# Kernel optimization log

Measured on AMD Instinct MI355X. Metric: run time of the kernel, lower is better.

## Reference

```python
import jax, jax.numpy as jnp
import numpy as np
import math

NUM_HEADS = 16
HEAD_DIM = 128
ROPE_BASE = 10000.0


def setup_inputs() -> dict:
    key = jax.random.key(0)
    ks = jax.random.split(key, 6)
    B, S, H = 2, 2048, 2048
    hidden_states = jax.random.normal(ks[0], (B, S, H), dtype=jnp.float32) * 0.02
    # causal additive mask, shape (B, 1, S, S)
    neg = jnp.finfo(jnp.float32).min
    causal = jnp.where(jnp.tril(jnp.ones((S, S), dtype=bool)), 0.0, neg).astype(jnp.float32)
    attention_mask = jnp.broadcast_to(causal[None, None], (B, 1, S, S))
    position_ids = jnp.broadcast_to(jnp.arange(S, dtype=jnp.int64)[None], (B, S))
    scale = 1.0 / math.sqrt(H)
    Wq = jax.random.normal(ks[1], (H, H), dtype=jnp.float32) * scale
    Wk = jax.random.normal(ks[2], (H, H), dtype=jnp.float32) * scale
    Wv = jax.random.normal(ks[3], (H, H), dtype=jnp.float32) * scale
    Wo = jax.random.normal(ks[4], (H, H), dtype=jnp.float32) * scale
    return {"hidden_states": hidden_states, "attention_mask": attention_mask,
            "position_ids": position_ids, "Wq": Wq, "Wk": Wk, "Wv": Wv, "Wo": Wo}


def _rotate_half(x):
    x1, x2 = jnp.split(x, 2, axis=-1)
    return jnp.concatenate((-x2, x1), axis=-1)


def reference(hidden_states, attention_mask, position_ids, Wq, Wk, Wv, Wo):
    B, S, H = hidden_states.shape
    nh, hd = NUM_HEADS, HEAD_DIM

    def shape_heads(x):  # (B,S,H) -> (B,nh,S,hd)
        return x.reshape(B, S, nh, hd).transpose(0, 2, 1, 3)

    q = shape_heads(hidden_states @ Wq.T)
    k = shape_heads(hidden_states @ Wk.T)
    v = shape_heads(hidden_states @ Wv.T)

    kv_seq_len = S  # no past_key_value
    # rotary table: (kv_seq_len, hd)
    inv_freq = 1.0 / (ROPE_BASE ** (jnp.arange(0, hd, 2, dtype=jnp.float32) / hd))
    t = jnp.arange(kv_seq_len, dtype=jnp.float32)
    freqs = jnp.einsum('i,j->ij', t, inv_freq)
    emb = jnp.concatenate((freqs, freqs), axis=-1)
    # gather-based RoPE == table lookup at position_ids: (B,S,hd) -> (B,1,S,hd)
    cos = jnp.cos(emb)[position_ids][:, None]
    sin = jnp.sin(emb)[position_ids][:, None]

    q = q * cos + _rotate_half(q) * sin
    k = k * cos + _rotate_half(k) * sin

    scores = jnp.einsum('bhqd,bhkd->bhqk', q, k) / math.sqrt(hd)
    scores = scores + attention_mask
    scores = jnp.maximum(scores, jnp.finfo(scores.dtype).min)
    probs = jax.nn.softmax(scores.astype(jnp.float32), axis=-1).astype(q.dtype)
    attn = jnp.einsum('bhqk,bhkd->bhqd', probs, v)  # (B,nh,S,hd)
    attn = attn.transpose(0, 2, 1, 3).reshape(B, S, H)
    return attn @ Wo.T
```

## Files before the change

kernel.cpp:

```cpp
#include <hip/hip_runtime.h>
#include <hip/hip_bf16.h>
#include <cstdint>

#define SQ    2048
#define HDIM  2048
#define NH    16
#define HD    128
#define BATCH 2
#define MTOK  (BATCH*SQ)

typedef unsigned short u16;
typedef unsigned int   u32;
typedef __bf16 bf16x8 __attribute__((ext_vector_type(8)));
typedef float  f32x4  __attribute__((ext_vector_type(4)));
typedef float  f32x16 __attribute__((ext_vector_type(16)));
typedef unsigned short u16x4 __attribute__((ext_vector_type(4)));
typedef unsigned int   u32x4 __attribute__((ext_vector_type(4)));

__device__ __forceinline__ u16 f2b(float f) {
  union { float f; unsigned u; } v; v.f = f;
  return (u16)((v.u + 0x7fffu + ((v.u >> 16) & 1u)) >> 16);
}
__device__ __forceinline__ float b2f(u16 b) {
  union { unsigned u; float f; } v; v.u = ((unsigned)b) << 16;
  return v.f;
}

#define GLD_LDS16(gp, lp) __builtin_amdgcn_global_load_lds( \
    (const __attribute__((address_space(1))) uint32_t*)(gp), \
    (__attribute__((address_space(3))) uint32_t*)(lp), 16, 0, 0)

__device__ __forceinline__ f32x16 zero16() {
  f32x16 v;
#pragma unroll
  for (int i = 0; i < 16; ++i) v[i] = 0.f;
  return v;
}

__global__ __launch_bounds__(256) void conv_bf16(const float* __restrict__ in,
                                                 u16* __restrict__ out, int n4) {
  int i = blockIdx.x * 256 + threadIdx.x;
  if (i >= n4) return;
  float4 v = ((const float4*)in)[i];
  u16x4 o;
  o.x = f2b(v.x); o.y = f2b(v.y); o.z = f2b(v.z); o.w = f2b(v.w);
  *(u16x4*)(out + (size_t)i * 4) = o;
}

__global__ __launch_bounds__(256) void conv_w4(const float* __restrict__ w0,
                                               const float* __restrict__ w1,
                                               const float* __restrict__ w2,
                                               const float* __restrict__ w3,
                                               u16* o0, u16* o1, u16* o2, u16* o3) {
  int i = blockIdx.x * 256 + threadIdx.x;
  int sel = blockIdx.y;
  const float* in = sel == 0 ? w0 : sel == 1 ? w1 : sel == 2 ? w2 : w3;
  u16* out = sel == 0 ? o0 : sel == 1 ? o1 : sel == 2 ? o2 : o3;
  float4 v = ((const float4*)in)[i];
  u16x4 o;
  o.x = f2b(v.x); o.y = f2b(v.y); o.z = f2b(v.z); o.w = f2b(v.w);
  *(u16x4*)(out + (size_t)i * 4) = o;
}

__global__ void rope_table_k(float* __restrict__ ct, float* __restrict__ st) {
  int s = blockIdx.x, j = threadIdx.x;
  float invf = expf(-(float)j * (9.210340371976184f / 64.0f));
  float ang = (float)s * invf;
  ct[s * 64 + j] = cosf(ang);
  st[s * 64 + j] = sinf(ang);
}

__global__ __launch_bounds__(256) void rope_apply2(u16* __restrict__ Xq,
                                                   u16* __restrict__ Xk,
                                                   const float* __restrict__ ct,
                                                   const float* __restrict__ st) {
  u16* X = blockIdx.y ? Xk : Xq;
  int idx = blockIdx.x * 256 + threadIdx.x;
  int j = idx & 63;
  int row = idx >> 6;
  int s = row & (SQ - 1);
  size_t base = (size_t)row * HD;
  float x1 = b2f(X[base + j]), x2 = b2f(X[base + j + 64]);
  float c = ct[s * 64 + j], sn = st[s * 64 + j];
  X[base + j]      = f2b(x1 * c - x2 * sn);
  X[base + j + 64] = f2b(x2 * c + x1 * sn);
}

template<int BM, int OUT>
__global__ __launch_bounds__(512, 2)
void gemm8(const u16* __restrict__ A, const u16* __restrict__ W0,
           const u16* __restrict__ W1, const u16* __restrict__ W2,
           u16* __restrict__ oQ, u16* __restrict__ oK, u16* __restrict__ oV,
           float* __restrict__ oF) {
  constexpr int ALT = BM / 64;
  constexpr int TLT = ALT + 4;
  constexpr int MF  = BM / 32;
  constexpr int MPP = MF / 4;
  __shared__ u16 Asb[2][BM * 64];
  __shared__ u16 Bsb[2][256 * 64];
  const int tid = threadIdx.x, lane = tid & 63, w = tid >> 6;
  const int wm = w >> 2, wn = w & 3;
  const int gx = gridDim.x;
  const int lin = blockIdx.y * gx + blockIdx.x;
  const int cpx = (gx * gridDim.y) >> 3;
  const int swz = (lin & 7) * cpx + (lin >> 3);
  const int bx = swz % gx, by = swz / gx;
  const int m0 = by * BM;
  const int n0g = bx * 256;
  int sel; const u16* Bw; int nloc;
  if (OUT == 0) {
    sel = n0g >> 11;
    Bw = (sel == 0) ? W0 : (sel == 1) ? W1 : W2;
    nloc = n0g & 2047;
  } else {
    sel = 0; Bw = W0; nloc = n0g;
  }

  size_t aoff[ALT]; int aldso[ALT];
  size_t boff[4];   int bldso[4];
#pragma unroll
  for (int i = 0; i < ALT; ++i) {
    int c = i * 512 + tid, r = c >> 3, sl = c & 7;
    aoff[i] = (size_t)(m0 + r) * HDIM + ((sl ^ (r & 7)) * 8);
    aldso[i] = (i * 512 + w * 64) * 8;
  }
#pragma unroll
  for (int i = 0; i < 4; ++i) {
    int c = i * 512 + tid, r = c >> 3, sl = c & 7;
    boff[i] = (size_t)(nloc + r) * HDIM + ((sl ^ (r & 7)) * 8);
    bldso[i] = (i * 512 + w * 64) * 8;
  }
  auto stage = [&](int buf, int k0) {
#pragma unroll
    for (int i = 0; i < ALT; ++i) GLD_LDS16(A + aoff[i] + k0, &Asb[buf][aldso[i]]);
#pragma unroll
    for (int i = 0; i < 4; ++i) GLD_LDS16(Bw + boff[i] + k0, &Bsb[buf][bldso[i]]);
  };

  f32x4 acc[MF][4];
#pragma unroll
  for (int i = 0; i < MF; ++i)
#pragma unroll
    for (int j = 0; j < 4; ++j) acc[i][j] = (f32x4){0.f, 0.f, 0.f, 0.f};

  const int l15 = lane & 15, hi4 = lane >> 4;
  const int swr = (l15 & 7) << 4;

  stage(0, 0);

  const int NT = HDIM / 64;
  for (int t = 0; t < NT; ++t) {
    const int cur = t & 1;
    if (t + 1 < NT) {
      stage(cur ^ 1, (t + 1) * 64);
      if constexpr (BM == 256) asm volatile("s_waitcnt vmcnt(8)" ::: "memory");
      else                     asm volatile("s_waitcnt vmcnt(6)" ::: "memory");
    } else {
      asm volatile("s_waitcnt vmcnt(0)" ::: "memory");
    }
    __builtin_amdgcn_s_barrier();

    const char* Ab = (const char*)Asb[cur];
    const char* Bb = (const char*)Bsb[cur];

    bf16x8 bfr[4][2];
#pragma unroll
    for (int ni = 0; ni < 4; ++ni)
#pragma unroll
      for (int kk = 0; kk < 2; ++kk)
        bfr[ni][kk] = *(const bf16x8*)(Bb + (wn * 64 + ni * 16 + l15) * 128 +
                                       ((kk * 64 + hi4 * 16) ^ swr));
    bf16x8 afA[MPP][2], afB[MPP][2];
    auto lda = [&](bf16x8 (&dst)[MPP][2], int pp) {
#pragma unroll
      for (int j = 0; j < MPP; ++j)
#pragma unroll
        for (int kk = 0; kk < 2; ++kk)
          dst[j][kk] = *(const bf16x8*)(Ab + (wm * (BM / 2) + (pp * MPP + j) * 16 + l15) * 128 +
                                        ((kk * 64 + hi4 * 16) ^ swr));
    };
    auto mf = [&](bf16x8 (&af)[MPP][2], int pp) {
#pragma unroll
      for (int kk = 0; kk < 2; ++kk)
#pragma unroll
        for (int j = 0; j < MPP; ++j)
#pragma unroll
          for (int ni = 0; ni < 4; ++ni)
            acc[pp * MPP + j][ni] = __builtin_amdgcn_mfma_f32_16x16x32_bf16(
                af[j][kk], bfr[ni][kk], acc[pp * MPP + j][ni], 0, 0, 0);
    };

    lda(afA, 0);
    asm volatile("s_waitcnt lgkmcnt(0)" ::: "memory");
    __builtin_amdgcn_sched_barrier(0);
    lda(afB, 1);
    __builtin_amdgcn_s_setprio(1); mf(afA, 0); __builtin_amdgcn_s_setprio(0);
    asm volatile("s_waitcnt lgkmcnt(0)" ::: "memory");
    __builtin_amdgcn_sched_barrier(0);
    lda(afA, 2);
    __builtin_amdgcn_s_setprio(1); mf(afB, 1); __builtin_amdgcn_s_setprio(0);
    asm volatile("s_waitcnt lgkmcnt(0)" ::: "memory");
    __builtin_amdgcn_sched_barrier(0);
    lda(afB, 3);
    __builtin_amdgcn_s_setprio(1); mf(afA, 2); __builtin_amdgcn_s_setprio(0);
    asm volatile("s_waitcnt lgkmcnt(0)" ::: "memory");
    __builtin_amdgcn_sched_barrier(0);
    __builtin_amdgcn_s_setprio(1); mf(afB, 3); __builtin_amdgcn_s_setprio(0);
    __builtin_amdgcn_s_barrier();
  }

  const int cl = l15, rg = hi4 * 4;
#pragma unroll
  for (int mi = 0; mi < MF; ++mi) {
#pragma unroll
    for (int ni = 0; ni < 4; ++ni) {
      const int mb = m0 + wm * (BM / 2) + mi * 16 + rg;
      const int n = nloc + wn * 64 + ni * 16 + cl;
      if (OUT == 1) {
#pragma unroll
        for (int r = 0; r < 4; ++r)
          oF[(size_t)(mb + r) * HDIM + n] = acc[mi][ni][r];
      } else {
        const int h = n >> 7, d = n & 127;
        if (sel == 2) {
          const int b = mb >> 11, s = mb & (SQ - 1);
          u16x4 pk;
          pk.x = f2b(acc[mi][ni][0]); pk.y = f2b(acc[mi][ni][1]);
          pk.z = f2b(acc[mi][ni][2]); pk.w = f2b(acc[mi][ni][3]);
          *(u16x4*)&oV[((size_t)(b * NH + h) * HD + d) * SQ + s] = pk;
        } else {
          u16* O = sel ? oK : oQ;
#pragma unroll
          for (int r = 0; r < 4; ++r) {
            const int m = mb + r, b = m >> 11, s = m & (SQ - 1);
            O[((size_t)(b * NH + h) * SQ + s) * HD + d] = f2b(acc[mi][ni][r]);
          }
        }
      }
    }
  }
}

__device__ __forceinline__ void stage_kv(u16* ksb, u16* vsb,
                                         const u16* __restrict__ Kg,
                                         const u16* __restrict__ Vg,
                                         int kv0, int w, int lane) {
#pragma unroll
  for (int i = 0; i < 4; ++i) {
    int chunk = (w * 4 + i) * 64 + lane;
    int row = chunk >> 4, c16 = chunk & 15;
    int csrc = c16 ^ (row & 7);
    GLD_LDS16(Kg + (size_t)(kv0 + row) * HD + csrc * 8, ksb + (w * 4 + i) * 512);
  }
#pragma unroll
  for (int i = 0; i < 4; ++i) {
    int chunk = (w * 4 + i) * 64 + lane;
    int d = chunk >> 3, c8 = chunk & 7;
    int csrc = c8 ^ (d & 7);
    GLD_LDS16(Vg + (size_t)d * SQ + kv0 + csrc * 8, vsb + (w * 4 + i) * 512);
  }
}

#define MKPA(dst, P, off) { \
  u32 u0_, u1_, u2_, u3_; \
  asm("v_cvt_pk_bf16_f32 %0, %1, %2" : "=v"(u0_) : "v"(P[off + 0]), "v"(P[off + 1])); \
  asm("v_cvt_pk_bf16_f32 %0, %1, %2" : "=v"(u1_) : "v"(P[off + 2]), "v"(P[off + 3])); \
  asm("v_cvt_pk_bf16_f32 %0, %1, %2" : "=v"(u2_) : "v"(P[off + 4]), "v"(P[off + 5])); \
  asm("v_cvt_pk_bf16_f32 %0, %1, %2" : "=v"(u3_) : "v"(P[off + 6]), "v"(P[off + 7])); \
  u32 x0_ = (u32)__shfl_xor((int)u0_, 32, 64); \
  u32 x1_ = (u32)__shfl_xor((int)u1_, 32, 64); \
  u32 x2_ = (u32)__shfl_xor((int)u2_, 32, 64); \
  u32 x3_ = (u32)__shfl_xor((int)u3_, 32, 64); \
  u32x4 w_; \
  w_.x = hi ? x2_ : u0_; \
  w_.y = hi ? x3_ : u1_; \
  w_.z = hi ? u2_ : x0_; \
  w_.w = hi ? u3_ : x1_; \
  dst = __builtin_bit_cast(bf16x8, w_); \
}

#define PVD(oD, dblk) { \
  const int dr_ = (dblk) * 32 + l31; \
  const int sw_ = (dr_ & 7) << 4; \
  bf16x8 v0_ = *(const bf16x8*)(Vb + ((dr_ * 128 +  0 + hi * 16) ^ sw_)); \
  oD = __builtin_amdgcn_mfma_f32_32x32x16_bf16(pa[0], v0_, oD, 0, 0, 0); \
  bf16x8 v1_ = *(const bf16x8*)(Vb + ((dr_ * 128 + 32 + hi * 16) ^ sw_)); \
  oD = __builtin_amdgcn_mfma_f32_32x32x16_bf16(pa[1], v1_, oD, 0, 0, 0); \
  bf16x8 v2_ = *(const bf16x8*)(Vb + ((dr_ * 128 + 64 + hi * 16) ^ sw_)); \
  oD = __builtin_amdgcn_mfma_f32_32x32x16_bf16(pa[2], v2_, oD, 0, 0, 0); \
  bf16x8 v3_ = *(const bf16x8*)(Vb + ((dr_ * 128 + 96 + hi * 16) ^ sw_)); \
  oD = __builtin_amdgcn_mfma_f32_32x32x16_bf16(pa[3], v3_, oD, 0, 0, 0); \
}

__global__ __launch_bounds__(256, 2)
void flash_fwd2(const u16* __restrict__ Q, const u16* __restrict__ K,
                const u16* __restrict__ Vt, u16* __restrict__ Out) {
  __shared__ u16 Ks[2][64 * 128];
  __shared__ u16 Vs[2][128 * 64];
  const int tid = threadIdx.x, lane = tid & 63, w = tid >> 6;
  const int hi = lane >> 5, l31 = lane & 31;
  const int qt = 15 - (int)(blockIdx.x >> 5);
  const int bh = blockIdx.x & 31;
  const int q0 = qt * 128;
  const u16* Qg = Q + (size_t)bh * SQ * HD;
  const u16* Kg = K + (size_t)bh * SQ * HD;
  const u16* Vg = Vt + (size_t)bh * HD * SQ;
  const int qw = q0 + w * 32;
  const int qg = qw + l31;

  bf16x8 qf[8];
#pragma unroll
  for (int st = 0; st < 8; ++st)
    qf[st] = *(const bf16x8*)&Qg[(size_t)qg * HD + st * 16 + hi * 8];

  f32x16 o0 = zero16(), o1 = zero16(), o2 = zero16(), o3 = zero16();
  float lsum = 0.f;
  const float sL2E = 0.1275174446f;
  const int ktl = 2 * qt + 1;
  int cur = 0;

  stage_kv(Ks[0], Vs[0], Kg, Vg, 0, w, lane);

  for (int kt = 0; kt <= ktl; ++kt) {
    if (kt < ktl) {
      stage_kv(Ks[cur ^ 1], Vs[cur ^ 1], Kg, Vg, (kt + 1) * 64, w, lane);
      asm volatile("s_waitcnt vmcnt(8)" ::: "memory");
    } else {
      asm volatile("s_waitcnt vmcnt(0)" ::: "memory");
    }
    __builtin_amdgcn_s_barrier();

    const int kv0 = kt * 64;
    if (kv0 <= qw + 31) {
      const char* Kb = (const char*)Ks[cur];
      const char* Vb = (const char*)Vs[cur];
      f32x16 c0 = zero16(), c1 = zero16();
      const int kr0 = l31, kr1 = 32 + l31;
      const int sw0 = (kr0 & 7) << 4;
#pragma unroll
      for (int st = 0; st < 8; ++st) {
        bf16x8 k0 = *(const bf16x8*)(Kb + ((kr0 * 256 + st * 32 + hi * 16) ^ sw0));
        c0 = __builtin_amdgcn_mfma_f32_32x32x16_bf16(k0, qf[st], c0, 0, 0, 0);
        bf16x8 k1 = *(const bf16x8*)(Kb + ((kr1 * 256 + st * 32 + hi * 16) ^ sw0));
        c1 = __builtin_amdgcn_mfma_f32_32x32x16_bf16(k1, qf[st], c1, 0, 0, 0);
      }
      const bool needmask = (kv0 + 63 > qw);
      const int lim0 = qg - kv0, lim1 = lim0 - 32;
      if (needmask) {
#pragma unroll
        for (int r = 0; r < 16; ++r) {
          const int cr = (r & 3) + 8 * (r >> 2) + 4 * hi;
          float p0 = exp2f(c0[r] * sL2E);
          c0[r] = (cr <= lim0) ? p0 : 0.f;
          float p1 = exp2f(c1[r] * sL2E);
          c1[r] = (cr <= lim1) ? p1 : 0.f;
          lsum += c0[r] + c1[r];
        }
      } else {
#pragma unroll
        for (int r = 0; r < 16; ++r) {
          c0[r] = exp2f(c0[r] * sL2E);
          c1[r] = exp2f(c1[r] * sL2E);
          lsum += c0[r] + c1[r];
        }
      }
      bf16x8 pa[4];
      MKPA(pa[0], c0, 0); MKPA(pa[1], c0, 8);
      MKPA(pa[2], c1, 0); MKPA(pa[3], c1, 8);
      PVD(o0, 0) PVD(o1, 1) PVD(o2, 2) PVD(o3, 3)
    }
    __builtin_amdgcn_s_barrier();
    cur ^= 1;
  }

  float ltot = lsum + __shfl_xor(lsum, 32, 64);
  float invl = 1.f / ltot;
  const int b = bh >> 4, h = bh & 15;
#pragma unroll
  for (int g = 0; g < 4; ++g) {
#pragma unroll
    for (int j = 0; j < 4; ++j) {
      const int r = g * 4 + j;
      const int cr = g * 8 + 4 * hi + j;
      float inv = __shfl(invl, cr, 64);
      const int s = q0 + w * 32 + cr;
      size_t rb = ((size_t)(b * SQ + s)) * HDIM + h * HD;
      Out[rb +  0 + l31] = f2b(o0[r] * inv);
      Out[rb + 32 + l31] = f2b(o1[r] * inv);
      Out[rb + 64 + l31] = f2b(o2[r] * inv);
      Out[rb + 96 + l31] = f2b(o3[r] * inv);
    }
  }
}

extern "C" void kernel_launch(void* const* d_in, const int* in_sizes, int n_in,
                              void* d_out, int out_size, void* d_ws, size_t ws_size,
                              hipStream_t stream) {
  const float* hs = (const float*)d_in[0];
  const float* Wq = (const float*)d_in[3];
  const float* Wk = (const float*)d_in[4];
  const float* Wv = (const float*)d_in[5];
  const float* Wo = (const float*)d_in[6];

  char* ws = (char*)d_ws;
  u16* XB  = (u16*)(ws);
  u16* WQB = (u16*)(ws + (size_t)(16 << 20));
  u16* WKB = (u16*)(ws + (size_t)(24 << 20));
  u16* WVB = (u16*)(ws + (size_t)(32 << 20));
  u16* WOB = (u16*)(ws + (size_t)(40 << 20));
  u16* QR  = (u16*)(ws + (size_t)(48 << 20));
  u16* KR  = (u16*)(ws + (size_t)(64 << 20));
  u16* VT  = (u16*)(ws + (size_t)(80 << 20));
  u16* ATT = (u16*)(ws + (size_t)(96 << 20));
  float* CT = (float*)(ws + (size_t)(112 << 20));
  float* ST = (float*)(ws + (size_t)(112 << 20) + (1 << 19));

  conv_bf16<<<8192, 256, 0, stream>>>(hs, XB, 2097152);
  conv_w4<<<dim3(4096, 4), 256, 0, stream>>>(Wq, Wk, Wv, Wo, WQB, WKB, WVB, WOB);
  rope_table_k<<<SQ, 64, 0, stream>>>(CT, ST);

  gemm8<256, 0><<<dim3(24, 16), 512, 0, stream>>>(XB, WQB, WKB, WVB,
                                                  QR, KR, VT, nullptr);

  rope_apply2<<<dim3(16384, 2), 256, 0, stream>>>(QR, KR, CT, ST);

  flash_fwd2<<<512, 256, 0, stream>>>(QR, KR, VT, ATT);

  gemm8<128, 1><<<dim3(8, 32), 512, 0, stream>>>(ATT, WOB, nullptr, nullptr,
                                                 nullptr, nullptr, nullptr,
                                                 (float*)d_out);
}
```

Baseline: 291.2 us.

## Split GEMM tiles into half-buffers with four-phase staggered load/compute pipeline

Rewrites the GEMM main loop so the A and B tiles are each split into two halves in shared memory. Each K-step runs four phases, and every phase issues the global-to-LDS load for one half of the next tile while computing on one quadrant of the current tile. The aim is finer-grained overlap of memory traffic with MFMA work and more even spreading of vmcnt waits. In exchange it adds a barrier per phase and makes the waitcnt bookkeeping more complex.

```diff
diff --git a/kernel.cpp b/kernel.cpp
--- a/kernel.cpp
+++ b/kernel.cpp
@@ -88,16 +88,17 @@
 
 template<int BM, int OUT>
 __global__ __launch_bounds__(512, 2)
-void gemm8(const u16* __restrict__ A, const u16* __restrict__ W0,
-           const u16* __restrict__ W1, const u16* __restrict__ W2,
-           u16* __restrict__ oQ, u16* __restrict__ oK, u16* __restrict__ oV,
-           float* __restrict__ oF) {
-  constexpr int ALT = BM / 64;
-  constexpr int TLT = ALT + 4;
+void gemm8j(const u16* __restrict__ A, const u16* __restrict__ W0,
+            const u16* __restrict__ W1, const u16* __restrict__ W2,
+            u16* __restrict__ oQ, u16* __restrict__ oK, u16* __restrict__ oV,
+            float* __restrict__ oF) {
   constexpr int MF  = BM / 32;
-  constexpr int MPP = MF / 4;
-  __shared__ u16 Asb[2][BM * 64];
-  __shared__ u16 Bsb[2][256 * 64];
+  constexpr int MH  = MF / 2;
+  constexpr int WU  = BM / 4;
+  constexpr int WUS = (BM == 256) ? 6 : 5;
+  constexpr int ALH = BM / 128;
+  __shared__ u16 Ah[2][2][(BM / 2) * 64];
+  __shared__ u16 Bh[2][2][128 * 64];
   const int tid = threadIdx.x, lane = tid & 63, w = tid >> 6;
   const int wm = w >> 2, wn = w & 3;
   const int gx = gridDim.x;
@@ -116,25 +117,31 @@
     sel = 0; Bw = W0; nloc = n0g;
   }
 
-  size_t aoff[ALT]; int aldso[ALT];
-  size_t boff[4];   int bldso[4];
-#pragma unroll
-  for (int i = 0; i < ALT; ++i) {
-    int c = i * 512 + tid, r = c >> 3, sl = c & 7;
-    aoff[i] = (size_t)(m0 + r) * HDIM + ((sl ^ (r & 7)) * 8);
-    aldso[i] = (i * 512 + w * 64) * 8;
-  }
-#pragma unroll
-  for (int i = 0; i < 4; ++i) {
-    int c = i * 512 + tid, r = c >> 3, sl = c & 7;
-    boff[i] = (size_t)(nloc + r) * HDIM + ((sl ^ (r & 7)) * 8);
-    bldso[i] = (i * 512 + w * 64) * 8;
-  }
-  auto stage = [&](int buf, int k0) {
-#pragma unroll
-    for (int i = 0; i < ALT; ++i) GLD_LDS16(A + aoff[i] + k0, &Asb[buf][aldso[i]]);
-#pragma unroll
-    for (int i = 0; i < 4; ++i) GLD_LDS16(Bw + boff[i] + k0, &Bsb[buf][bldso[i]]);
+  u32 aoff[2][ALH], boff[2][2];
+#pragma unroll
+  for (int h = 0; h < 2; ++h) {
+#pragma unroll
+    for (int l = 0; l < ALH; ++l) {
+      int c = l * 512 + tid, ra = c >> 3, sl = c & 7;
+      int r = ((ra >> WUS) << (WUS + 1)) + h * WU + (ra & (WU - 1));
+      aoff[h][l] = (u32)((m0 + r) * HDIM + ((sl ^ (ra & 7)) * 8));
+    }
+#pragma unroll
+    for (int l = 0; l < 2; ++l) {
+      int c = l * 512 + tid, cb = c >> 3, sl = c & 7;
+      int col = nloc + ((cb >> 5) * 64) + h * 32 + (cb & 31);
+      boff[h][l] = (u32)(col * HDIM + ((sl ^ (cb & 7)) * 8));
+    }
+  }
+  auto stageA = [&](int buf, int h, int k0) {
+#pragma unroll
+    for (int l = 0; l < ALH; ++l)
+      GLD_LDS16(A + (size_t)aoff[h][l] + k0, &Ah[buf][h][(l * 512 + tid) * 8]);
+  };
+  auto stageB = [&](int buf, int h, int k0) {
+#pragma unroll
+    for (int l = 0; l < 2; ++l)
+      GLD_LDS16(Bw + (size_t)boff[h][l] + k0, &Bh[buf][h][(l * 512 + tid) * 8]);
   };
 
   f32x4 acc[MF][4];
@@ -146,67 +153,89 @@
   const int l15 = lane & 15, hi4 = lane >> 4;
   const int swr = (l15 & 7) << 4;
 
-  stage(0, 0);
+  stageA(0, 0, 0); stageB(0, 0, 0); stageA(0, 1, 0); stageB(0, 1, 0);
+  if constexpr (BM == 256) asm volatile("s_waitcnt vmcnt(4)" ::: "memory");
+  else                     asm volatile("s_waitcnt vmcnt(3)" ::: "memory");
+  __builtin_amdgcn_s_barrier();
+
+  bf16x8 bfv[2][2][2];
+  bf16x8 afv[MH][2];
 
   const int NT = HDIM / 64;
   for (int t = 0; t < NT; ++t) {
-    const int cur = t & 1;
-    if (t + 1 < NT) {
-      stage(cur ^ 1, (t + 1) * 64);
-      if constexpr (BM == 256) asm volatile("s_waitcnt vmcnt(8)" ::: "memory");
-      else                     asm volatile("s_waitcnt vmcnt(6)" ::: "memory");
-    } else {
-      asm volatile("s_waitcnt vmcnt(0)" ::: "memory");
-    }
-    __builtin_amdgcn_s_barrier();
-
-    const char* Ab = (const char*)Asb[cur];
-    const char* Bb = (const char*)Bsb[cur];
-
-    bf16x8 bfr[4][2];
-#pragma unroll
-    for (int ni = 0; ni < 4; ++ni)
+    const int cur = t & 1, nb = cur ^ 1;
+    const bool st = (t + 1 < NT);
+    const int kn = (t + 1) * 64;
+    const char* Ab0 = (const char*)&Ah[cur][0][0];
+    const char* Ab1 = (const char*)&Ah[cur][1][0];
+    const char* Bb0 = (const char*)&Bh[cur][0][0];
+    const char* Bb1 = (const char*)&Bh[cur][1][0];
+
+#pragma unroll
+    for (int p = 0; p < 4; ++p) {
+      const int mh = p >> 1, nh = p & 1;
+      if (p == 0) {
+#pragma unroll
+        for (int j2 = 0; j2 < 2; ++j2)
+#pragma unroll
+          for (int kk = 0; kk < 2; ++kk)
+            bfv[0][j2][kk] = *(const bf16x8*)(Bb0 + (wn * 32 + j2 * 16 + l15) * 128 +
+                                              ((kk * 64 + hi4 * 16) ^ swr));
+#pragma unroll
+        for (int j = 0; j < MH; ++j)
+#pragma unroll
+          for (int kk = 0; kk < 2; ++kk)
+            afv[j][kk] = *(const bf16x8*)(Ab0 + (wm * WU + j * 16 + l15) * 128 +
+                                          ((kk * 64 + hi4 * 16) ^ swr));
+      } else if (p == 1) {
+#pragma unroll
+        for (int j2 = 0; j2 < 2; ++j2)
+#pragma unroll
+          for (int kk = 0; kk < 2; ++kk)
+            bfv[1][j2][kk] = *(const bf16x8*)(Bb1 + (wn * 32 + j2 * 16 + l15) * 128 +
+                                              ((kk * 64 + hi4 * 16) ^ swr));
+      } else if (p == 2) {
+#pragma unroll
+        for (int j = 0; j < MH; ++j)
+#pragma unroll
+          for (int kk = 0; kk < 2; ++kk)
+            afv[j][kk] = *(const bf16x8*)(Ab1 + (wm * WU + j * 16 + l15) * 128 +
+                                          ((kk * 64 + hi4 * 16) ^ swr));
+      }
+      if (st) {
+        if (p == 0) stageA(nb, 0, kn);
+        else if (p == 1) stageB(nb, 0, kn);
+        else if (p == 2) stageA(nb, 1, kn);
+        else stageB(nb, 1, kn);
+      }
+      if (p == 0) {
+        if (st) {
+          if constexpr (BM == 256) asm volatile("s_waitcnt vmcnt(2)" ::: "memory");
+          else                     asm volatile("s_waitcnt vmcnt(1)" ::: "memory");
+        } else {
+          asm volatile("s_waitcnt vmcnt(0)" ::: "memory");
+        }
+        if constexpr (BM == 256) asm volatile("s_waitcnt lgkmcnt(8)" ::: "memory");
+      }
+      if (p == 3 && st) {
+        if constexpr (BM == 256) asm volatile("s_waitcnt vmcnt(4)" ::: "memory");
+        else                     asm volatile("s_waitcnt vmcnt(3)" ::: "memory");
+      }
+      __builtin_amdgcn_s_barrier();
+      asm volatile("s_waitcnt lgkmcnt(0)" ::: "memory");
+      __builtin_amdgcn_sched_barrier(0);
+      __builtin_amdgcn_s_setprio(1);
 #pragma unroll
       for (int kk = 0; kk < 2; ++kk)
-        bfr[ni][kk] = *(const bf16x8*)(Bb + (wn * 64 + ni * 16 + l15) * 128 +
-                                       ((kk * 64 + hi4 * 16) ^ swr));
-    bf16x8 afA[MPP][2], afB[MPP][2];
-    auto lda = [&](bf16x8 (&dst)[MPP][2], int pp) {
-#pragma unroll
-      for (int j = 0; j < MPP; ++j)
-#pragma unroll
-        for (int kk = 0; kk < 2; ++kk)
-          dst[j][kk] = *(const bf16x8*)(Ab + (wm * (BM / 2) + (pp * MPP + j) * 16 + l15) * 128 +
-                                        ((kk * 64 + hi4 * 16) ^ swr));
-    };
-    auto mf = [&](bf16x8 (&af)[MPP][2], int pp) {
-#pragma unroll
-      for (int kk = 0; kk < 2; ++kk)
-#pragma unroll
-        for (int j = 0; j < MPP; ++j)
-#pragma unroll
-          for (int ni = 0; ni < 4; ++ni)
-            acc[pp * MPP + j][ni] = __builtin_amdgcn_mfma_f32_16x16x32_bf16(
-                af[j][kk], bfr[ni][kk], acc[pp * MPP + j][ni], 0, 0, 0);
-    };
-
-    lda(afA, 0);
-    asm volatile("s_waitcnt lgkmcnt(0)" ::: "memory");
-    __builtin_amdgcn_sched_barrier(0);
-    lda(afB, 1);
-    __builtin_amdgcn_s_setprio(1); mf(afA, 0); __builtin_amdgcn_s_setprio(0);
-    asm volatile("s_waitcnt lgkmcnt(0)" ::: "memory");
-    __builtin_amdgcn_sched_barrier(0);
-    lda(afA, 2);
-    __builtin_amdgcn_s_setprio(1); mf(afB, 1); __builtin_amdgcn_s_setprio(0);
-    asm volatile("s_waitcnt lgkmcnt(0)" ::: "memory");
-    __builtin_amdgcn_sched_barrier(0);
-    lda(afB, 3);
-    __builtin_amdgcn_s_setprio(1); mf(afA, 2); __builtin_amdgcn_s_setprio(0);
-    asm volatile("s_waitcnt lgkmcnt(0)" ::: "memory");
-    __builtin_amdgcn_sched_barrier(0);
-    __builtin_amdgcn_s_setprio(1); mf(afB, 3); __builtin_amdgcn_s_setprio(0);
-    __builtin_amdgcn_s_barrier();
+#pragma unroll
+        for (int j = 0; j < MH; ++j)
+#pragma unroll
+          for (int j2 = 0; j2 < 2; ++j2)
+            acc[mh * MH + j][nh * 2 + j2] = __builtin_amdgcn_mfma_f32_16x16x32_bf16(
+                afv[j][kk], bfv[nh][j2][kk], acc[mh * MH + j][nh * 2 + j2], 0, 0, 0);
+      __builtin_amdgcn_s_setprio(0);
+      __builtin_amdgcn_s_barrier();
+    }
   }
 
   const int cl = l15, rg = hi4 * 4;
@@ -419,14 +448,14 @@
   conv_w4<<<dim3(4096, 4), 256, 0, stream>>>(Wq, Wk, Wv, Wo, WQB, WKB, WVB, WOB);
   rope_table_k<<<SQ, 64, 0, stream>>>(CT, ST);
 
-  gemm8<256, 0><<<dim3(24, 16), 512, 0, stream>>>(XB, WQB, WKB, WVB,
-                                                  QR, KR, VT, nullptr);
+  gemm8j<256, 0><<<dim3(24, 16), 512, 0, stream>>>(XB, WQB, WKB, WVB,
+                                                   QR, KR, VT, nullptr);
 
   rope_apply2<<<dim3(16384, 2), 256, 0, stream>>>(QR, KR, CT, ST);
 
   flash_fwd2<<<512, 256, 0, stream>>>(QR, KR, VT, ATT);
 
-  gemm8<128, 1><<<dim3(8, 32), 512, 0, stream>>>(ATT, WOB, nullptr, nullptr,
-                                                 nullptr, nullptr, nullptr,
-                                                 (float*)d_out);
-}
+  gemm8j<128, 1><<<dim3(8, 32), 512, 0, stream>>>(ATT, WOB, nullptr, nullptr,
+                                                  nullptr, nullptr, nullptr,
+                                                  (float*)d_out);
+}
```

New measurement: 276.1 us. 1.05x faster.
